# Optimization experiments

Hardware: AMD Instinct MI355X
Metric: run time of the kernel (lower is better)

Reference implementation:

```python
import jax, jax.numpy as jnp
import numpy as np
import math

B, S, DIM, QK, HID = 20, 500, 300, 128, 600  # batch, seq, model dim, query_key_dim, hidden_dim
ROT = 32          # rotary dim = min(32, query_key_dim)
NB, MD = 32, 128  # T5 bias num_buckets, max_distance


def _layernorm(x, g, b, eps=1e-5):
    mu = jnp.mean(x, axis=-1, keepdims=True)
    var = jnp.var(x, axis=-1, keepdims=True)
    return (x - mu) / jnp.sqrt(var + eps) * g + b


def _rowquant(y, axis):
    # per-row (or per-col) symmetric int4-range quant used by the module:
    # scale = max|y|/15, clamp to [-15,15], truncate toward zero (torch .to(int8))
    s = jnp.max(jnp.abs(y), axis=axis, keepdims=True) / 15.0
    yq = jnp.trunc(jnp.clip(y / s, -15.0, 15.0))
    return yq, s


def _rotary(t):
    # rotary-embedding-torch: rotate first ROT features, interleaved pairs
    inv_freq = 1.0 / (10000.0 ** (jnp.arange(0, ROT, 2, dtype=jnp.float32) / ROT))  # [ROT/2]
    pos = jnp.arange(S, dtype=jnp.float32)
    freqs = jnp.repeat(pos[:, None] * inv_freq[None, :], 2, axis=-1)  # [S, ROT]
    cos, sin = jnp.cos(freqs), jnp.sin(freqs)
    tr, tp = t[..., :ROT], t[..., ROT:]
    x1, x2 = tr[..., 0::2], tr[..., 1::2]
    rot_half = jnp.stack([-x2, x1], axis=-1).reshape(tr.shape)
    return jnp.concatenate([tr * cos + rot_half * sin, tp], axis=-1)


def _t5_bias(rel_emb):
    # non-causal T5 relative position bucket, num_buckets=32 -> halved to 16
    pos = jnp.arange(S)
    n = -(pos[None, :] - pos[:, None])  # -(k_pos - q_pos)
    nb = NB // 2
    ret = (n < 0).astype(jnp.int32) * nb
    n = jnp.abs(n)
    max_exact = nb // 2
    is_small = n < max_exact
    n_safe = jnp.maximum(n, 1).astype(jnp.float32)
    val_large = max_exact + (jnp.log(n_safe / max_exact) / math.log(MD / max_exact) * (nb - max_exact)).astype(jnp.int32)
    val_large = jnp.minimum(val_large, nb - 1)
    bucket = ret + jnp.where(is_small, n, val_large)  # [S, S]
    return rel_emb[bucket, 0] * math.sqrt(QK)


def setup_inputs() -> dict:
    key = jax.random.key(0)
    ks = jax.random.split(key, 16)
    nrm = lambda i, shp, std=0.02: jax.random.normal(ks[i], shp, jnp.float32) * std
    uni = lambda i, shp, lo, hi: jax.random.uniform(ks[i], shp, jnp.float32, lo, hi)
    return {
        "x": jax.random.normal(ks[0], (B, S, DIM), jnp.float32),
        "norm_gamma": jnp.ones((DIM,), jnp.float32),
        "norm_beta": jnp.zeros((DIM,), jnp.float32),
        "Wh": nrm(1, (2 * HID, DIM)),
        "bh": jnp.zeros((2 * HID,), jnp.float32),
        "Wqk": nrm(2, (QK, DIM)),
        "bqk": jnp.zeros((QK,), jnp.float32),
        "os_gamma": nrm(3, (2, QK)),
        "os_beta": jnp.zeros((2, QK), jnp.float32),
        "Wo": nrm(4, (DIM, HID)),
        "bo": jnp.zeros((DIM,), jnp.float32),
        "rel_emb": nrm(5, (NB, 1), 0.1),
        "qk_s": uni(6, (DIM,), 0.5, 1.5),
        "hidden_s": uni(7, (DIM,), 0.5, 1.5),
        "out_s": uni(8, (HID,), 0.5, 1.5),
        "hidden_params": uni(9, (2 * HID,), 0.01, 0.05),
        "qk_params": uni(10, (QK,), 0.01, 0.05),
        "out_params": uni(11, (DIM,), 0.01, 0.05),
    }


def reference(x, norm_gamma, norm_beta, Wh, bh, Wqk, bqk, os_gamma, os_beta, Wo, bo,
              rel_emb, qk_s, hidden_s, out_s, hidden_params, qk_params, out_params):
    normed = _layernorm(x, norm_gamma, norm_beta)
    # token shift on first half of features
    half = DIM // 2
    x_shift = jnp.pad(normed[..., :half], ((0, 0), (1, 0), (0, 0)))[:, :S, :]
    normed = jnp.concatenate([x_shift, normed[..., half:]], axis=-1)

    # per-weight-column pre-scale then per-row int8 quant
    xq_q, sq = _rowquant(normed / qk_s, axis=-1)      # sq [B,S,1]
    xh_q, sh = _rowquant(normed / hidden_s, axis=-1)  # sh [B,S,1]

    # to_hidden: Linear + SiLU, then dequant outer(row_scale, hidden_params)
    v_gate = jax.nn.silu(xh_q @ Wh.T + bh) * (sh * hidden_params)  # [B,S,2*HID]
    v, gate = v_gate[..., :HID], v_gate[..., HID:]

    qk = jax.nn.silu(xq_q @ Wqk.T + bqk) * (sq * qk_params)  # [B,S,QK]
    q = qk * os_gamma[0] + os_beta[0]
    k = qk * os_gamma[1] + os_beta[1]
    q, k = _rotary(q), _rotary(k)

    qq, qs = _rowquant(q, axis=-1)
    kq, ks_ = _rowquant(k, axis=-1)
    sim = jnp.trunc(jnp.einsum('bid,bjd->bij', qq, kq)) * qs * jnp.swapaxes(ks_, 1, 2)
    sim = sim + _t5_bias(rel_emb)

    attn = jnp.square(jax.nn.relu(sim / S))
    aq, as_ = _rowquant(attn, axis=-1)  # as_ [B,S,1]
    vq, vs = _rowquant(v, axis=1)       # vs [B,1,HID] (per-column)
    out = jnp.trunc(jnp.einsum('bij,bjd->bid', aq, vq)) * as_ * vs  # [B,S,HID]

    out = out * gate / out_s
    oq, osc = _rowquant(out, axis=-1)
    out = (oq @ Wo.T + bo) * (osc * out_params)  # [B,S,DIM]
    return out + x
```

## Files before the change

### kernel.cpp

```cpp
#include <hip/hip_runtime.h>
#include <math.h>

#define B_   20
#define S_   500
#define DIM_ 300
#define QK_  128
#define HID_ 600
#define NROW (B_ * S_)

typedef int   v4i  __attribute__((ext_vector_type(4)));

__device__ __forceinline__ unsigned short f32_to_bf16(float f) {
  unsigned int u = __float_as_uint(f);
  unsigned int r = (u + 0x7FFFu + ((u >> 16) & 1u)) >> 16;
  return (unsigned short)r;
}
__device__ __forceinline__ float bf16_to_f32(unsigned short s) {
  return __uint_as_float(((unsigned int)s) << 16);
}

__device__ __forceinline__ float quant15(float y, float s) {
  return truncf(fminf(fmaxf(__fdiv_rn(y, s), -15.f), 15.f));
}

__global__ __launch_bounds__(256) void k_prep_ln(
    const float* __restrict__ x,
    const float* __restrict__ g, const float* __restrict__ b,
    const float* __restrict__ qk_s, const float* __restrict__ hidden_s,
    signed char* __restrict__ xq8, signed char* __restrict__ xh8,
    float* __restrict__ sq, float* __restrict__ sh,
    const float* __restrict__ rel_emb, float* __restrict__ dbias,
    const float* __restrict__ Wh, signed char* __restrict__ q1h, float* __restrict__ s1h,
    const float* __restrict__ Wo, signed char* __restrict__ q1o, float* __restrict__ s1o,
    const float* __restrict__ Wqk, signed char* __restrict__ q1k, float* __restrict__ s1k) {
  int blk = blockIdx.x;
  int tid = threadIdx.x;
  int lane = tid & 63;
  if (blk < 2500) {
    int row = blk * 4 + (tid >> 6);
    if (row >= NROW) return;
    bool hasp = (row % S_) > 0;
    const float* xr = x + (size_t)row * DIM_;
    const float* xpr = x + (size_t)(row - 1) * DIM_;
    float xc[5], xp[5];
    #pragma unroll
    for (int i = 0; i < 5; ++i) {
      int c = lane + i * 64;
      xc[i] = (c < DIM_) ? xr[c] : 0.f;
      xp[i] = (hasp && c < DIM_) ? xpr[c] : 0.f;
    }
    float sc = 0.f, sp = 0.f;
    #pragma unroll
    for (int i = 0; i < 5; ++i) { sc += xc[i]; sp += xp[i]; }
    #pragma unroll
    for (int off = 1; off < 64; off <<= 1) {
      sc += __shfl_xor(sc, off);
      sp += __shfl_xor(sp, off);
    }
    float mu_c = sc / (float)DIM_, mu_p = sp / (float)DIM_;
    float vc = 0.f, vp = 0.f;
    #pragma unroll
    for (int i = 0; i < 5; ++i) {
      int c = lane + i * 64;
      if (c < DIM_) {
        float dc = xc[i] - mu_c; vc += dc * dc;
        float dp = xp[i] - mu_p; vp += dp * dp;
      }
    }
    #pragma unroll
    for (int off = 1; off < 64; off <<= 1) {
      vc += __shfl_xor(vc, off);
      vp += __shfl_xor(vp, off);
    }
    float den_c = sqrtf(vc / (float)DIM_ + 1e-5f);
    float den_p = sqrtf(vp / (float)DIM_ + 1e-5f);
    float yq[5], yh[5];
    float mq = 0.f, mh = 0.f;
    #pragma unroll
    for (int i = 0; i < 5; ++i) {
      int c = lane + i * 64;
      if (c < DIM_) {
        float src;
        if (c < DIM_ / 2)
          src = hasp ? __fdiv_rn(xp[i] - mu_p, den_p) * g[c] + b[c] : 0.f;
        else
          src = __fdiv_rn(xc[i] - mu_c, den_c) * g[c] + b[c];
        yq[i] = __fdiv_rn(src, qk_s[c]);
        yh[i] = __fdiv_rn(src, hidden_s[c]);
        mq = fmaxf(mq, fabsf(yq[i]));
        mh = fmaxf(mh, fabsf(yh[i]));
      }
    }
    #pragma unroll
    for (int off = 1; off < 64; off <<= 1) {
      mq = fmaxf(mq, __shfl_xor(mq, off));
      mh = fmaxf(mh, __shfl_xor(mh, off));
    }
    float sqv = mq / 15.0f, shv = mh / 15.0f;
    if (lane == 0) { sq[row] = sqv; sh[row] = shv; }
    #pragma unroll
    for (int i = 0; i < 5; ++i) {
      int c = lane + i * 64;
      if (c < DIM_) {
        xq8[(size_t)row * 320 + c] = (signed char)quant15(yq[i], sqv);
        xh8[(size_t)row * 320 + c] = (signed char)quant15(yh[i], shv);
      } else if (c < 320) {
        xq8[(size_t)row * 320 + c] = 0;
        xh8[(size_t)row * 320 + c] = 0;
      }
    }
    return;
  }
  int jidx = (blk - 2500) * 4 + (tid >> 6);
  if (jidx >= 1744) return;
  if (jidx < 16) {
    int idx = jidx * 64 + lane;
    int dd = idx - 512;
    int ret = (dd < 0) ? 16 : 0;
    int n = dd < 0 ? -dd : dd;
    int v;
    if (n < 8)       v = n;
    else if (n < 12) v = 8;
    else if (n < 16) v = 9;
    else if (n < 23) v = 10;
    else if (n < 32) v = 11;
    else if (n < 46) v = 12;
    else if (n < 64) v = 13;
    else if (n < 91) v = 14;
    else             v = 15;
    dbias[idx] = __fmul_rn(rel_emb[ret + v], 11.313708498984761f);
    return;
  }
  const float* src; signed char* q1; float* s1;
  int j, C, CP;
  if (jidx < 1296)      { j = jidx - 16;   src = Wh;  q1 = q1h; s1 = s1h; C = DIM_; CP = 320; }
  else if (jidx < 1616) { j = jidx - 1296; src = Wo;  q1 = q1o; s1 = s1o; C = HID_; CP = 640; }
  else                  { j = jidx - 1616; src = Wqk; q1 = q1k; s1 = s1k; C = DIM_; CP = 320; }
  float m = 0.f;
  for (int k = lane; k < C; k += 64) m = fmaxf(m, fabsf(src[(size_t)j * C + k]));
  #pragma unroll
  for (int off = 1; off < 64; off <<= 1) m = fmaxf(m, __shfl_xor(m, off));
  float s1v = m / 127.0f;
  float s1inv = s1v > 0.f ? 1.0f / s1v : 0.f;
  if (lane == 0) s1[j] = s1v;
  for (int k = lane; k < CP; k += 64) {
    float wv = (k < C) ? src[(size_t)j * C + k] : 0.f;
    float q1f = fminf(fmaxf(rintf(wv * s1inv), -127.f), 127.f);
    q1[(size_t)j * CP + k] = (signed char)q1f;
  }
}

__global__ __launch_bounds__(512) void k_hqk(
    const signed char* __restrict__ xh8p, const signed char* __restrict__ xq8p,
    const float* __restrict__ sh, const float* __restrict__ sq,
    const signed char* __restrict__ q1h, const float* __restrict__ s1h,
    const float* __restrict__ bh, const float* __restrict__ hp,
    unsigned short* __restrict__ v16, unsigned short* __restrict__ gate16,
    int* __restrict__ vsmax,
    const signed char* __restrict__ q1k, const float* __restrict__ s1k,
    const float* __restrict__ bqk, const float* __restrict__ qkp,
    const float* __restrict__ osg, const float* __restrict__ osb,
    signed char* __restrict__ qq8, signed char* __restrict__ kq2,
    float* __restrict__ qs, float* __restrict__ ks) {
  __shared__ __align__(16) signed char smem[33792];
  int blk = blockIdx.x;
  int tid = threadIdx.x;
  int w = tid >> 6, l = tid & 63, g = l >> 4, ln = l & 15;
  v4i zero = {0, 0, 0, 0};
  int rxor = ((g ^ ((ln >> 1) & 3)) * 16);

  if (blk < 760) {
    int j0 = (blk % 19) * 64;
    int i0 = (blk / 19) * 256;
    int wm = w >> 1, wn = w & 1;
    signed char* a_lds  = smem;
    signed char* b1_lds = smem + 16384;
    unsigned short* st  = (unsigned short*)smem;

    int r0 = tid >> 2, ch0 = tid & 3;
    int r1 = r0 + 128;
    int koff0 = ((ch0 ^ ((r0 >> 1) & 3)) * 16);
    int koff1 = ((ch0 ^ ((r1 >> 1) & 3)) * 16);
    int ga0 = i0 + r0; if (ga0 >= NROW) ga0 = NROW - 1;
    int ga1 = i0 + r1; if (ga1 >= NROW) ga1 = NROW - 1;
    const signed char* srcA0 = xh8p + (size_t)ga0 * 320 + koff0;
    const signed char* srcA1 = xh8p + (size_t)ga1 * 320 + koff1;
    bool hasB = tid < 256;
    int br = (tid & 255) >> 2, bch = tid & 3;
    int bkoff = ((bch ^ ((br >> 1) & 3)) * 16);
    const signed char* srcB = q1h + (size_t)(j0 + br) * 320 + bkoff;

    v4i pa0 = *(const v4i*)srcA0;
    v4i pa1 = *(const v4i*)srcA1;
    v4i pb = hasB ? *(const v4i*)srcB : zero;

    v4i acc1[4][2];
    #pragma unroll
    for (int sl = 0; sl < 4; ++sl)
      #pragma unroll
      for (int t = 0; t < 2; ++t) acc1[sl][t] = zero;

    for (int st_i = 0; st_i < 5; ++st_i) {
      *(v4i*)(a_lds + tid * 16)        = pa0;
      *(v4i*)(a_lds + 8192 + tid * 16) = pa1;
      if (hasB) *(v4i*)(b1_lds + tid * 16) = pb;
      __syncthreads();
      if (st_i < 4) {
        int k0 = (st_i + 1) * 64;
        pa0 = *(const v4i*)(srcA0 + k0);
        pa1 = *(const v4i*)(srcA1 + k0);
        if (hasB) pb = *(const v4i*)(srcB + k0);
      }
      v4i af[4];
      #pragma unroll
      for (int sl = 0; sl < 4; ++sl)
        af[sl] = *(const v4i*)(a_lds + (wm * 64 + sl * 16 + ln) * 64 + rxor);
      #pragma unroll
      for (int t = 0; t < 2; ++t) {
        int boff = (wn * 32 + t * 16 + ln) * 64 + rxor;
        v4i b1 = *(const v4i*)(b1_lds + boff);
        #pragma unroll
        for (int sl = 0; sl < 4; ++sl)
          acc1[sl][t] = __builtin_amdgcn_mfma_i32_16x16x64_i8(af[sl], b1, acc1[sl][t], 0, 0, 0);
      }
      __syncthreads();
    }
    int rbase = i0 + wm * 64;
    int b0 = rbase / S_;
    int bbound = (b0 + 1) * S_;
    int rtop = rbase + 63; if (rtop >= NROW) rtop = NROW - 1;
    int b1i = rtop / S_;
    #pragma unroll
    for (int t = 0; t < 2; ++t) {
      int col = j0 + wn * 32 + t * 16 + ln;
      int cl = wn * 32 + t * 16 + ln;
      if (col < 2 * HID_) {
        float s1v = s1h[col], bc = bh[col], hpc = hp[col];
        bool isv = col < HID_;
        float m0 = 0.f, m1 = 0.f;
        #pragma unroll
        for (int sl = 0; sl < 4; ++sl) {
          #pragma unroll
          for (int r = 0; r < 4; ++r) {
            int grow = rbase + sl * 16 + g * 4 + r;
            if (grow < NROW) {
              float z = s1v * (float)acc1[sl][t][r] + bc;
              float sig = 1.0f / (1.0f + __expf(-z));
              float val = __fmul_rn(z * sig, __fmul_rn(sh[grow], hpc));
              unsigned short hv = f32_to_bf16(val);
              st[(wm * 64 + sl * 16 + g * 4 + r) * 66 + cl] = hv;
              if (isv) {
                float vr = fabsf(bf16_to_f32(hv));
                if (grow < bbound) m0 = fmaxf(m0, vr);
                else               m1 = fmaxf(m1, vr);
              }
            }
          }
        }
        if (isv) {
          atomicMax(&vsmax[b0 * 640 + col], __float_as_int(m0));
          if (b1i != b0) atomicMax(&vsmax[b1i * 640 + col], __float_as_int(m1));
        }
      }
    }
    __syncthreads();
    for (int idx = tid; idx < 2048; idx += 512) {
      int r = idx >> 3, seg = idx & 7;
      int grow = i0 + r;
      int col0 = j0 + seg * 8;
      if (grow < NROW && col0 < 2 * HID_) {
        const unsigned int* sp = (const unsigned int*)(st + r * 66 + seg * 8);
        v4i pk;
        pk[0] = sp[0]; pk[1] = sp[1]; pk[2] = sp[2]; pk[3] = sp[3];
        if (col0 < HID_)
          *(v4i*)(v16 + (size_t)grow * HID_ + col0) = pk;
        else
          *(v4i*)(gate16 + (size_t)grow * HID_ + (col0 - HID_)) = pk;
      }
    }
    return;
  }
  {
    int i0 = (blk - 760) * 128;
    signed char* a_lds  = smem;
    signed char* b1_lds = smem + 8192;
    float* freqs = (float*)(smem + 16384);
    if (tid < 32) {
      double e = (double)(tid & ~1) / 32.0;
      freqs[tid] = (float)(1.0 / pow(10000.0, e));
    }
    int r = tid >> 2, ch = tid & 3;
    int koff = ((ch ^ ((r >> 1) & 3)) * 16);
    int ga = i0 + r; if (ga >= NROW) ga = NROW - 1;
    const signed char* srcA  = xq8p + (size_t)ga * 320 + koff;
    const signed char* srcB1 = q1k + (size_t)r * 320 + koff;
    v4i pa  = *(const v4i*)srcA;
    v4i pb1 = *(const v4i*)srcB1;
    v4i acc1[8];
    #pragma unroll
    for (int t = 0; t < 8; ++t) acc1[t] = zero;
    for (int st = 0; st < 5; ++st) {
      *(v4i*)(a_lds + tid * 16)  = pa;
      *(v4i*)(b1_lds + tid * 16) = pb1;
      __syncthreads();
      if (st < 4) {
        int k0 = (st + 1) * 64;
        pa  = *(const v4i*)(srcA + k0);
        pb1 = *(const v4i*)(srcB1 + k0);
      }
      v4i af = *(const v4i*)(a_lds + (w * 16 + ln) * 64 + rxor);
      #pragma unroll
      for (int t = 0; t < 8; ++t) {
        int boff = (t * 16 + ln) * 64 + rxor;
        v4i b1 = *(const v4i*)(b1_lds + boff);
        acc1[t] = __builtin_amdgcn_mfma_i32_16x16x64_i8(af, b1, acc1[t], 0, 0, 0);
      }
      __syncthreads();
    }
    int growr[4]; float sqr[4];
    #pragma unroll
    for (int r2 = 0; r2 < 4; ++r2) {
      growr[r2] = i0 + w * 16 + g * 4 + r2;
      int gc = growr[r2] < NROW ? growr[r2] : NROW - 1;
      sqr[r2] = sq[gc];
    }
    float qv[8][4], kv[8][4];
    #pragma unroll
    for (int t = 0; t < 8; ++t) {
      int c = t * 16 + ln;
      float s1v = s1k[c], bc = bqk[c], qkpc = qkp[c];
      float g0 = osg[c], g1 = osg[QK_ + c], b0 = osb[c], b1v = osb[QK_ + c];
      #pragma unroll
      for (int r2 = 0; r2 < 4; ++r2) {
        float z = s1v * (float)acc1[t][r2] + bc;
        float sig = 1.0f / (1.0f + expf(-z));
        float qkv = __fmul_rn(z * sig, __fmul_rn(sqr[r2], qkpc));
        qv[t][r2] = __fadd_rn(__fmul_rn(qkv, g0), b0);
        kv[t][r2] = __fadd_rn(__fmul_rn(qkv, g1), b1v);
      }
    }
    #pragma unroll
    for (int t = 0; t < 2; ++t) {
      float inv = freqs[t * 16 + ln];
      #pragma unroll
      for (int r2 = 0; r2 < 4; ++r2) {
        int pos = growr[r2] % S_;
        float fr = __fmul_rn((float)pos, inv);
        float cs = cosf(fr), sn = sinf(fr);
        float qo = __shfl_xor(qv[t][r2], 1);
        float ko = __shfl_xor(kv[t][r2], 1);
        float rq = ((ln & 1) == 0) ? -qo : qo;
        float rk = ((ln & 1) == 0) ? -ko : ko;
        qv[t][r2] = __fadd_rn(__fmul_rn(qv[t][r2], cs), __fmul_rn(rq, sn));
        kv[t][r2] = __fadd_rn(__fmul_rn(kv[t][r2], cs), __fmul_rn(rk, sn));
      }
    }
    float qsv[4], ksv[4];
    #pragma unroll
    for (int r2 = 0; r2 < 4; ++r2) {
      float mq = 0.f, mk = 0.f;
      #pragma unroll
      for (int t = 0; t < 8; ++t) {
        mq = fmaxf(mq, fabsf(qv[t][r2]));
        mk = fmaxf(mk, fabsf(kv[t][r2]));
      }
      #pragma unroll
      for (int off = 1; off < 16; off <<= 1) {
        mq = fmaxf(mq, __shfl_xor(mq, off));
        mk = fmaxf(mk, __shfl_xor(mk, off));
      }
      qsv[r2] = mq / 15.0f; ksv[r2] = mk / 15.0f;
      if (ln == 0 && growr[r2] < NROW) { qs[growr[r2]] = qsv[r2]; ks[growr[r2]] = ksv[r2]; }
    }
    #pragma unroll
    for (int t = 0; t < 8; ++t) {
      int c = t * 16 + ln;
      #pragma unroll
      for (int r2 = 0; r2 < 4; ++r2) {
        if (growr[r2] < NROW) {
          qq8[(size_t)growr[r2] * QK_ + c] = (signed char)quant15(qv[t][r2], qsv[r2]);
          int bb = growr[r2] / S_, ss = growr[r2] % S_;
          kq2[(((size_t)bb * 2 + (c >> 6)) * 512 + ss) * 64 + (c & 63)] =
              (signed char)quant15(kv[t][r2], ksv[r2]);
        }
      }
    }
  }
}

__global__ __launch_bounds__(512) void k_simpv(
    const signed char* __restrict__ qq8, const signed char* __restrict__ kq2,
    const float* __restrict__ qs, const float* __restrict__ ks,
    const float* __restrict__ dbias,
    const signed char* __restrict__ vqt2, const float* __restrict__ vg,
    const unsigned short* __restrict__ gate16,
    signed char* __restrict__ oq8, float* __restrict__ osc) {
  int i0 = blockIdx.x * 16;
  int b = blockIdx.y;
  int tid = threadIdx.x;
  int w = tid >> 6, l = tid & 63, g = l >> 4, ln = l & 15;
  __shared__ __align__(16) signed char q_lds[16 * 144];
  __shared__ __align__(16) signed char p_lds[16 * 528];
  __shared__ float db[1024];
  __shared__ int rowmax[16];
  if (tid < 128) {
    int r = tid >> 3, ww = tid & 7;
    *(v4i*)(q_lds + r * 144 + ww * 16) =
        *(const v4i*)(qq8 + ((size_t)(b * S_ + i0 + r)) * QK_ + ww * 16);
  }
  for (int idx = tid; idx < 1024; idx += 512) db[idx] = dbias[idx];
  if (tid < 16) rowmax[tid] = 0;
  __syncthreads();
  v4i acc[4];
  v4i zero = {0, 0, 0, 0};
  #pragma unroll
  for (int t = 0; t < 4; ++t) acc[t] = zero;
  #pragma unroll
  for (int kk = 0; kk < 2; ++kk) {
    v4i afrag = *(const v4i*)(q_lds + ln * 144 + kk * 64 + g * 16);
    #pragma unroll
    for (int t = 0; t < 4; ++t) {
      int j0 = (w * 4 + t) * 16;
      v4i bfrag = *(const v4i*)(kq2 + (((size_t)b * 2 + kk) * 512 + j0 + ln) * 64 + g * 16);
      acc[t] = __builtin_amdgcn_mfma_i32_16x16x64_i8(afrag, bfrag, acc[t], 0, 0, 0);
    }
  }
  float qsr[4];
  #pragma unroll
  for (int r = 0; r < 4; ++r) qsr[r] = qs[b * S_ + i0 + g * 4 + r];
  float rm[4] = {0.f, 0.f, 0.f, 0.f};
  #pragma unroll
  for (int t = 0; t < 4; ++t) {
    int j = (w * 4 + t) * 16 + ln;
    bool jv = j < S_;
    float ksv = ks[b * S_ + j];
    #pragma unroll
    for (int r = 0; r < 4; ++r) {
      int ip = i0 + g * 4 + r;
      float av = 0.f;
      if (jv) {
        float simv = __fmul_rn(__fmul_rn((float)acc[t][r], qsr[r]), ksv);
        simv = __fadd_rn(simv, db[ip - j + 512]);
        float rr = fmaxf(__fmul_rn(simv, 0.002f), 0.f);
        av = __fmul_rn(rr, rr);
      }
      rm[r] = fmaxf(rm[r], av);
      acc[t][r] = __float_as_int(av);
    }
  }
  #pragma unroll
  for (int r = 0; r < 4; ++r) atomicMax(&rowmax[g * 4 + r], __float_as_int(rm[r]));
  __syncthreads();
  float asr[4], rinv[4];
  #pragma unroll
  for (int r = 0; r < 4; ++r) {
    asr[r] = __int_as_float(rowmax[g * 4 + r]) / 15.0f;
    rinv[r] = __fdiv_rn(1.0f, asr[r]);
  }
  #pragma unroll
  for (int t = 0; t < 4; ++t) {
    int j = (w * 4 + t) * 16 + ln;
    #pragma unroll
    for (int r = 0; r < 4; ++r) {
      float y = __int_as_float(acc[t][r]);
      float q = truncf(fminf(fmaxf(__fmul_rn(y, rinv[r]), -15.f), 15.f));
      p_lds[(g * 4 + r) * 528 + j] = (signed char)q;
    }
  }
  __syncthreads();
  if (tid < 16) rowmax[tid] = 0;
  __syncthreads();
  v4i pacc[5];
  #pragma unroll
  for (int t = 0; t < 5; ++t) pacc[t] = zero;
  for (int kk = 0; kk < 8; ++kk) {
    v4i afrag = *(const v4i*)(p_lds + ln * 528 + kk * 64 + g * 16);
    const signed char* bbase = vqt2 + (((size_t)b * 8 + kk) * 640) * 64 + g * 16;
    #pragma unroll
    for (int t = 0; t < 5; ++t) {
      int d = (w * 5 + t) * 16 + ln;
      v4i bfrag = *(const v4i*)(bbase + (size_t)d * 64);
      pacc[t] = __builtin_amdgcn_mfma_i32_16x16x64_i8(afrag, bfrag, pacc[t], 0, 0, 0);
    }
  }
  float rm2[4] = {0.f, 0.f, 0.f, 0.f};
  #pragma unroll
  for (int t = 0; t < 5; ++t) {
    int d = (w * 5 + t) * 16 + ln;
    bool dv = d < HID_;
    float vgv = vg[b * 640 + d];
    #pragma unroll
    for (int r = 0; r < 4; ++r) {
      float o = 0.f;
      if (dv) {
        float gt = bf16_to_f32(gate16[((size_t)(b * S_ + i0 + g * 4 + r)) * HID_ + d]);
        o = __fmul_rn(__fmul_rn(__fmul_rn((float)pacc[t][r], asr[r]), vgv), gt);
      }
      rm2[r] = fmaxf(rm2[r], fabsf(o));
      pacc[t][r] = __float_as_int(o);
    }
  }
  #pragma unroll
  for (int r = 0; r < 4; ++r) atomicMax(&rowmax[g * 4 + r], __float_as_int(rm2[r]));
  __syncthreads();
  float orinv[4];
  #pragma unroll
  for (int r = 0; r < 4; ++r) {
    float osr = __int_as_float(rowmax[g * 4 + r]) / 15.0f;
    orinv[r] = __fdiv_rn(1.0f, osr);
  }
  #pragma unroll
  for (int t = 0; t < 5; ++t) {
    int d = (w * 5 + t) * 16 + ln;
    #pragma unroll
    for (int r = 0; r < 4; ++r) {
      int il = i0 + g * 4 + r;
      if (il < S_) {
        signed char valc = 0;
        if (d < HID_) {
          float q = truncf(fminf(fmaxf(
              __fmul_rn(__int_as_float(pacc[t][r]), orinv[r]), -15.f), 15.f));
          valc = (signed char)q;
        }
        oq8[((size_t)b * S_ + il) * 640 + d] = valc;
      }
    }
  }
  if (tid < 16 && i0 + tid < S_)
    osc[b * S_ + i0 + tid] = __int_as_float(rowmax[tid]) / 15.0f;
}

__global__ __launch_bounds__(256) void k_vq2(const unsigned short* __restrict__ v16,
                                             const int* __restrict__ vsmax,
                                             const float* __restrict__ out_s,
                                             signed char* __restrict__ vqt2,
                                             float* __restrict__ vg) {
  int b = blockIdx.z;
  int s0 = blockIdx.x * 64;
  int d0 = blockIdx.y * 64;
  __shared__ float tile[64][65];
  int tid = threadIdx.x;
  int dj = tid & 63, si4 = tid >> 6;
  #pragma unroll
  for (int it = 0; it < 16; ++it) {
    int s = s0 + it * 4 + si4;
    int d = d0 + dj;
    float val = 0.f;
    if (s < S_ && d < HID_) val = bf16_to_f32(v16[((size_t)b * S_ + s) * HID_ + d]);
    tile[it * 4 + si4][dj] = val;
  }
  if (blockIdx.x == 0 && tid < 64) {
    int d = d0 + tid;
    float vsv = __int_as_float(vsmax[b * 640 + d]) / 15.0f;
    vg[b * 640 + d] = (d < HID_) ? __fdiv_rn(vsv, out_s[d]) : 0.f;
  }
  __syncthreads();
  int dd = tid >> 2, seg = tid & 3;
  int d = d0 + dd;
  int kk = s0 >> 6;
  v4i pack = {0, 0, 0, 0};
  if (d < HID_) {
    float vsv = __int_as_float(vsmax[b * 640 + d]) / 15.0f;
    signed char* pc = (signed char*)&pack;
    #pragma unroll
    for (int e = 0; e < 16; ++e)
      pc[e] = (signed char)quant15(tile[seg * 16 + e][dd], vsv);
  }
  *(v4i*)(vqt2 + ((((size_t)b * 8 + kk) * 640) + d) * 64 + seg * 16) = pack;
}

__global__ __launch_bounds__(256) void k_final(
    const signed char* __restrict__ oq8p, const float* __restrict__ osc,
    const signed char* __restrict__ q1o, const float* __restrict__ s1o,
    const float* __restrict__ bo, const float* __restrict__ op,
    const float* __restrict__ x, float* __restrict__ out) {
  int i0 = blockIdx.x * 128;
  int j0 = blockIdx.y * 64;
  int tid = threadIdx.x;
  int w = tid >> 6, l = tid & 63, g = l >> 4, ln = l & 15;
  int wm = w >> 1, wn = w & 1;
  __shared__ __align__(16) signed char a_lds[128 * 64];
  __shared__ __align__(16) signed char b1_lds[64 * 64];

  int arow0 = tid >> 2;
  int xorb = (((tid & 3) ^ ((tid >> 3) & 3)) * 16);
  int ga0 = i0 + arow0;       if (ga0 >= NROW) ga0 = NROW - 1;
  int ga1 = i0 + arow0 + 64;  if (ga1 >= NROW) ga1 = NROW - 1;
  int gcol = j0 + arow0;
  const signed char* srcA0 = oq8p + (size_t)ga0 * 640 + xorb;
  const signed char* srcA1 = oq8p + (size_t)ga1 * 640 + xorb;
  const signed char* srcB1 = q1o + (size_t)gcol * 640 + xorb;

  v4i pa0 = *(const v4i*)(srcA0);
  v4i pa1 = *(const v4i*)(srcA1);
  v4i pb1 = *(const v4i*)(srcB1);

  int rxor = ((g ^ ((ln >> 1) & 3)) * 16);
  v4i acc1[4][2];
  v4i zero = {0, 0, 0, 0};
  #pragma unroll
  for (int sl = 0; sl < 4; ++sl)
    #pragma unroll
    for (int t = 0; t < 2; ++t) acc1[sl][t] = zero;

  for (int st = 0; st < 10; ++st) {
    *(v4i*)(a_lds + tid * 16)        = pa0;
    *(v4i*)(a_lds + 4096 + tid * 16) = pa1;
    *(v4i*)(b1_lds + tid * 16)       = pb1;
    __syncthreads();
    if (st < 9) {
      int k0 = (st + 1) * 64;
      pa0 = *(const v4i*)(srcA0 + k0);
      pa1 = *(const v4i*)(srcA1 + k0);
      pb1 = *(const v4i*)(srcB1 + k0);
    }
    v4i af[4];
    #pragma unroll
    for (int sl = 0; sl < 4; ++sl)
      af[sl] = *(const v4i*)(a_lds + (wm * 64 + sl * 16 + ln) * 64 + rxor);
    #pragma unroll
    for (int t = 0; t < 2; ++t) {
      int boff = (wn * 32 + t * 16 + ln) * 64 + rxor;
      v4i b1 = *(const v4i*)(b1_lds + boff);
      #pragma unroll
      for (int sl = 0; sl < 4; ++sl)
        acc1[sl][t] = __builtin_amdgcn_mfma_i32_16x16x64_i8(af[sl], b1, acc1[sl][t], 0, 0, 0);
    }
    __syncthreads();
  }
  #pragma unroll
  for (int t = 0; t < 2; ++t) {
    int col = j0 + wn * 32 + t * 16 + ln;
    if (col < DIM_) {
      float s1v = s1o[col], bc = bo[col], opc = op[col];
      #pragma unroll
      for (int sl = 0; sl < 4; ++sl) {
        #pragma unroll
        for (int r = 0; r < 4; ++r) {
          int grow = i0 + wm * 64 + sl * 16 + g * 4 + r;
          if (grow < NROW) {
            float z = s1v * (float)acc1[sl][t][r] + bc;
            float tval = __fmul_rn(osc[grow], opc);
            out[(size_t)grow * DIM_ + col] =
                __fmul_rn(z, tval) + x[(size_t)grow * DIM_ + col];
          }
        }
      }
    }
  }
}

extern "C" void kernel_launch(void* const* d_in, const int* in_sizes, int n_in,
                              void* d_out, int out_size, void* d_ws, size_t ws_size,
                              hipStream_t stream) {
  const float* x        = (const float*)d_in[0];
  const float* ng       = (const float*)d_in[1];
  const float* nbt      = (const float*)d_in[2];
  const float* Wh       = (const float*)d_in[3];
  const float* bh       = (const float*)d_in[4];
  const float* Wqk      = (const float*)d_in[5];
  const float* bqk      = (const float*)d_in[6];
  const float* osg      = (const float*)d_in[7];
  const float* osb      = (const float*)d_in[8];
  const float* Wo       = (const float*)d_in[9];
  const float* bo       = (const float*)d_in[10];
  const float* rel      = (const float*)d_in[11];
  const float* qk_s     = (const float*)d_in[12];
  const float* hidden_s = (const float*)d_in[13];
  const float* out_s    = (const float*)d_in[14];
  const float* hp       = (const float*)d_in[15];
  const float* qkp      = (const float*)d_in[16];
  const float* op       = (const float*)d_in[17];
  float* out = (float*)d_out;

  char* ws = (char*)d_ws;
  size_t off = 0;
  auto alloc = [&](size_t bytes) {
    void* p = ws + off;
    off += (bytes + 255) & ~(size_t)255;
    return p;
  };
  signed char* xq8    = (signed char*)alloc((size_t)(NROW + 128) * 320);
  signed char* xh8    = (signed char*)alloc((size_t)(NROW + 256) * 320);
  float*       sq     = (float*)      alloc((size_t)(NROW + 256) * 4);
  float*       sh     = (float*)      alloc((size_t)(NROW + 256) * 4);
  unsigned short* v16   = (unsigned short*)alloc((size_t)(NROW + 256) * HID_ * 2);
  unsigned short* gate16= (unsigned short*)alloc((size_t)(NROW + 256) * HID_ * 2);
  signed char* qq8    = (signed char*)alloc((size_t)(NROW + 128) * QK_);
  signed char* kq2    = (signed char*)alloc((size_t)B_ * 2 * 512 * 64);
  float*       qs     = (float*)      alloc((size_t)(NROW + 128) * 4);
  float*       ks     = (float*)      alloc((size_t)(NROW + 128) * 4);
  signed char* vqt2   = (signed char*)alloc((size_t)B_ * 8 * 640 * 64);
  float*       vg     = (float*)      alloc((size_t)B_ * 640 * 4);
  int*         vsmax  = (int*)        alloc((size_t)B_ * 640 * 4);
  signed char* oq8    = (signed char*)alloc((size_t)(NROW + 128) * 640);
  float*       osc    = (float*)      alloc((size_t)(NROW + 128) * 4);
  float*       dbias  = (float*)      alloc((size_t)1024 * 4);
  signed char* q1h    = (signed char*)alloc((size_t)1280 * 320);
  float*       s1h    = (float*)      alloc((size_t)1280 * 4);
  signed char* q1o    = (signed char*)alloc((size_t)320 * 640);
  float*       s1o    = (float*)      alloc((size_t)320 * 4);
  signed char* q1k    = (signed char*)alloc((size_t)QK_ * 320);
  float*       s1k    = (float*)      alloc((size_t)QK_ * 4);


  k_prep_ln<<<2936, 256, 0, stream>>>(x, ng, nbt, qk_s, hidden_s, xq8, xh8, sq, sh,
                                      rel, dbias, Wh, q1h, s1h, Wo, q1o, s1o,
                                      Wqk, q1k, s1k);
  k_hqk<<<839, 512, 0, stream>>>(xh8, xq8, sh, sq, q1h, s1h, bh, hp,
                                 v16, gate16, vsmax,
                                 q1k, s1k, bqk, qkp, osg, osb,
                                 qq8, kq2, qs, ks);
  k_vq2<<<dim3(8, 10, B_), 256, 0, stream>>>(v16, vsmax, out_s, vqt2, vg);
  k_simpv<<<dim3(32, B_), 512, 0, stream>>>(qq8, kq2, qs, ks, dbias, vqt2, vg,
                                            gate16, oq8, osc);
  k_final<<<dim3(79, 5), 256, 0, stream>>>(oq8, osc, q1o, s1o, bo, op, x, out);
}
```

Baseline: 128.6 us.

## Split fused hidden/QK projection kernel into separate launches with smaller QK tiles

The combined k_hqk kernel, which branched on block index between the hidden projection and the QK projection, is split into two kernels. k_hidden keeps the 256x64 tile on a 2D grid. k_qk now uses 64-row tiles with 256 threads and 157 blocks instead of 79 blocks of 128 rows, which gives the QK path more parallelism and uses less LDS per block. The cost is an extra kernel launch and the loss of running both branches concurrently inside one grid.

```diff
diff --git a/kernel.cpp b/kernel.cpp
--- a/kernel.cpp
+++ b/kernel.cpp
@@ -150,239 +150,242 @@
   }
 }
 
-__global__ __launch_bounds__(512) void k_hqk(
-    const signed char* __restrict__ xh8p, const signed char* __restrict__ xq8p,
-    const float* __restrict__ sh, const float* __restrict__ sq,
+__global__ __launch_bounds__(512) void k_hidden(
+    const signed char* __restrict__ xh8p, const float* __restrict__ sh,
     const signed char* __restrict__ q1h, const float* __restrict__ s1h,
     const float* __restrict__ bh, const float* __restrict__ hp,
     unsigned short* __restrict__ v16, unsigned short* __restrict__ gate16,
-    int* __restrict__ vsmax,
+    int* __restrict__ vsmax) {
+  int j0 = blockIdx.x * 64;
+  int i0 = blockIdx.y * 256;
+  int tid = threadIdx.x;
+  int w = tid >> 6, l = tid & 63, g = l >> 4, ln = l & 15;
+  int wm = w >> 1, wn = w & 1;
+  __shared__ __align__(16) signed char smem[33792];
+  signed char* a_lds  = smem;
+  signed char* b1_lds = smem + 16384;
+  unsigned short* st  = (unsigned short*)smem;
+
+  int r0 = tid >> 2, ch0 = tid & 3;
+  int r1 = r0 + 128;
+  int koff0 = ((ch0 ^ ((r0 >> 1) & 3)) * 16);
+  int koff1 = ((ch0 ^ ((r1 >> 1) & 3)) * 16);
+  int ga0 = i0 + r0; if (ga0 >= NROW) ga0 = NROW - 1;
+  int ga1 = i0 + r1; if (ga1 >= NROW) ga1 = NROW - 1;
+  const signed char* srcA0 = xh8p + (size_t)ga0 * 320 + koff0;
+  const signed char* srcA1 = xh8p + (size_t)ga1 * 320 + koff1;
+  bool hasB = tid < 256;
+  int br = (tid & 255) >> 2, bch = tid & 3;
+  int bkoff = ((bch ^ ((br >> 1) & 3)) * 16);
+  const signed char* srcB = q1h + (size_t)(j0 + br) * 320 + bkoff;
+
+  v4i pa0 = *(const v4i*)srcA0;
+  v4i pa1 = *(const v4i*)srcA1;
+  v4i zero = {0, 0, 0, 0};
+  v4i pb = hasB ? *(const v4i*)srcB : zero;
+
+  int rxor = ((g ^ ((ln >> 1) & 3)) * 16);
+  v4i acc1[4][2];
+  #pragma unroll
+  for (int sl = 0; sl < 4; ++sl)
+    #pragma unroll
+    for (int t = 0; t < 2; ++t) acc1[sl][t] = zero;
+
+  for (int st_i = 0; st_i < 5; ++st_i) {
+    *(v4i*)(a_lds + tid * 16)        = pa0;
+    *(v4i*)(a_lds + 8192 + tid * 16) = pa1;
+    if (hasB) *(v4i*)(b1_lds + tid * 16) = pb;
+    __syncthreads();
+    if (st_i < 4) {
+      int k0 = (st_i + 1) * 64;
+      pa0 = *(const v4i*)(srcA0 + k0);
+      pa1 = *(const v4i*)(srcA1 + k0);
+      if (hasB) pb = *(const v4i*)(srcB + k0);
+    }
+    v4i af[4];
+    #pragma unroll
+    for (int sl = 0; sl < 4; ++sl)
+      af[sl] = *(const v4i*)(a_lds + (wm * 64 + sl * 16 + ln) * 64 + rxor);
+    #pragma unroll
+    for (int t = 0; t < 2; ++t) {
+      int boff = (wn * 32 + t * 16 + ln) * 64 + rxor;
+      v4i b1 = *(const v4i*)(b1_lds + boff);
+      #pragma unroll
+      for (int sl = 0; sl < 4; ++sl)
+        acc1[sl][t] = __builtin_amdgcn_mfma_i32_16x16x64_i8(af[sl], b1, acc1[sl][t], 0, 0, 0);
+    }
+    __syncthreads();
+  }
+  int rbase = i0 + wm * 64;
+  int b0 = rbase / S_;
+  int bbound = (b0 + 1) * S_;
+  int rtop = rbase + 63; if (rtop >= NROW) rtop = NROW - 1;
+  int b1i = rtop / S_;
+  #pragma unroll
+  for (int t = 0; t < 2; ++t) {
+    int col = j0 + wn * 32 + t * 16 + ln;
+    int cl = wn * 32 + t * 16 + ln;
+    if (col < 2 * HID_) {
+      float s1v = s1h[col], bc = bh[col], hpc = hp[col];
+      bool isv = col < HID_;
+      float m0 = 0.f, m1 = 0.f;
+      #pragma unroll
+      for (int sl = 0; sl < 4; ++sl) {
+        #pragma unroll
+        for (int r = 0; r < 4; ++r) {
+          int grow = rbase + sl * 16 + g * 4 + r;
+          if (grow < NROW) {
+            float z = s1v * (float)acc1[sl][t][r] + bc;
+            float sig = 1.0f / (1.0f + __expf(-z));
+            float val = __fmul_rn(z * sig, __fmul_rn(sh[grow], hpc));
+            unsigned short hv = f32_to_bf16(val);
+            st[(wm * 64 + sl * 16 + g * 4 + r) * 66 + cl] = hv;
+            if (isv) {
+              float vr = fabsf(bf16_to_f32(hv));
+              if (grow < bbound) m0 = fmaxf(m0, vr);
+              else               m1 = fmaxf(m1, vr);
+            }
+          }
+        }
+      }
+      if (isv) {
+        atomicMax(&vsmax[b0 * 640 + col], __float_as_int(m0));
+        if (b1i != b0) atomicMax(&vsmax[b1i * 640 + col], __float_as_int(m1));
+      }
+    }
+  }
+  __syncthreads();
+  for (int idx = tid; idx < 2048; idx += 512) {
+    int r = idx >> 3, seg = idx & 7;
+    int grow = i0 + r;
+    int col0 = j0 + seg * 8;
+    if (grow < NROW && col0 < 2 * HID_) {
+      const unsigned int* sp = (const unsigned int*)(st + r * 66 + seg * 8);
+      v4i pk;
+      pk[0] = sp[0]; pk[1] = sp[1]; pk[2] = sp[2]; pk[3] = sp[3];
+      if (col0 < HID_)
+        *(v4i*)(v16 + (size_t)grow * HID_ + col0) = pk;
+      else
+        *(v4i*)(gate16 + (size_t)grow * HID_ + (col0 - HID_)) = pk;
+    }
+  }
+}
+
+__global__ __launch_bounds__(256) void k_qk(
+    const signed char* __restrict__ xq8p, const float* __restrict__ sq,
     const signed char* __restrict__ q1k, const float* __restrict__ s1k,
     const float* __restrict__ bqk, const float* __restrict__ qkp,
     const float* __restrict__ osg, const float* __restrict__ osb,
     signed char* __restrict__ qq8, signed char* __restrict__ kq2,
     float* __restrict__ qs, float* __restrict__ ks) {
-  __shared__ __align__(16) signed char smem[33792];
-  int blk = blockIdx.x;
+  int i0 = blockIdx.x * 64;
   int tid = threadIdx.x;
   int w = tid >> 6, l = tid & 63, g = l >> 4, ln = l & 15;
+  __shared__ __align__(16) signed char a_lds[64 * 64];
+  __shared__ __align__(16) signed char b1_lds[128 * 64];
+  __shared__ float freqs[32];
+  if (tid < 32) {
+    double e = (double)(tid & ~1) / 32.0;
+    freqs[tid] = (float)(1.0 / pow(10000.0, e));
+  }
+  int arow = tid >> 2;
+  int xorb = (((tid & 3) ^ ((tid >> 3) & 3)) * 16);
+  int ga = i0 + arow; if (ga >= NROW) ga = NROW - 1;
+  const signed char* srcA   = xq8p + (size_t)ga * 320 + xorb;
+  const signed char* srcB1a = q1k + (size_t)arow * 320 + xorb;
+  const signed char* srcB1b = q1k + (size_t)(64 + arow) * 320 + xorb;
+  v4i pa   = *(const v4i*)srcA;
+  v4i pb1a = *(const v4i*)srcB1a, pb1b = *(const v4i*)srcB1b;
+  int rxor = ((g ^ ((ln >> 1) & 3)) * 16);
+  v4i acc1[8];
   v4i zero = {0, 0, 0, 0};
-  int rxor = ((g ^ ((ln >> 1) & 3)) * 16);
-
-  if (blk < 760) {
-    int j0 = (blk % 19) * 64;
-    int i0 = (blk / 19) * 256;
-    int wm = w >> 1, wn = w & 1;
-    signed char* a_lds  = smem;
-    signed char* b1_lds = smem + 16384;
-    unsigned short* st  = (unsigned short*)smem;
-
-    int r0 = tid >> 2, ch0 = tid & 3;
-    int r1 = r0 + 128;
-    int koff0 = ((ch0 ^ ((r0 >> 1) & 3)) * 16);
-    int koff1 = ((ch0 ^ ((r1 >> 1) & 3)) * 16);
-    int ga0 = i0 + r0; if (ga0 >= NROW) ga0 = NROW - 1;
-    int ga1 = i0 + r1; if (ga1 >= NROW) ga1 = NROW - 1;
-    const signed char* srcA0 = xh8p + (size_t)ga0 * 320 + koff0;
-    const signed char* srcA1 = xh8p + (size_t)ga1 * 320 + koff1;
-    bool hasB = tid < 256;
-    int br = (tid & 255) >> 2, bch = tid & 3;
-    int bkoff = ((bch ^ ((br >> 1) & 3)) * 16);
-    const signed char* srcB = q1h + (size_t)(j0 + br) * 320 + bkoff;
-
-    v4i pa0 = *(const v4i*)srcA0;
-    v4i pa1 = *(const v4i*)srcA1;
-    v4i pb = hasB ? *(const v4i*)srcB : zero;
-
-    v4i acc1[4][2];
-    #pragma unroll
-    for (int sl = 0; sl < 4; ++sl)
-      #pragma unroll
-      for (int t = 0; t < 2; ++t) acc1[sl][t] = zero;
-
-    for (int st_i = 0; st_i < 5; ++st_i) {
-      *(v4i*)(a_lds + tid * 16)        = pa0;
-      *(v4i*)(a_lds + 8192 + tid * 16) = pa1;
-      if (hasB) *(v4i*)(b1_lds + tid * 16) = pb;
-      __syncthreads();
-      if (st_i < 4) {
-        int k0 = (st_i + 1) * 64;
-        pa0 = *(const v4i*)(srcA0 + k0);
-        pa1 = *(const v4i*)(srcA1 + k0);
-        if (hasB) pb = *(const v4i*)(srcB + k0);
-      }
-      v4i af[4];
-      #pragma unroll
-      for (int sl = 0; sl < 4; ++sl)
-        af[sl] = *(const v4i*)(a_lds + (wm * 64 + sl * 16 + ln) * 64 + rxor);
-      #pragma unroll
-      for (int t = 0; t < 2; ++t) {
-        int boff = (wn * 32 + t * 16 + ln) * 64 + rxor;
-        v4i b1 = *(const v4i*)(b1_lds + boff);
-        #pragma unroll
-        for (int sl = 0; sl < 4; ++sl)
-          acc1[sl][t] = __builtin_amdgcn_mfma_i32_16x16x64_i8(af[sl], b1, acc1[sl][t], 0, 0, 0);
-      }
-      __syncthreads();
-    }
-    int rbase = i0 + wm * 64;
-    int b0 = rbase / S_;
-    int bbound = (b0 + 1) * S_;
-    int rtop = rbase + 63; if (rtop >= NROW) rtop = NROW - 1;
-    int b1i = rtop / S_;
-    #pragma unroll
-    for (int t = 0; t < 2; ++t) {
-      int col = j0 + wn * 32 + t * 16 + ln;
-      int cl = wn * 32 + t * 16 + ln;
-      if (col < 2 * HID_) {
-        float s1v = s1h[col], bc = bh[col], hpc = hp[col];
-        bool isv = col < HID_;
-        float m0 = 0.f, m1 = 0.f;
-        #pragma unroll
-        for (int sl = 0; sl < 4; ++sl) {
-          #pragma unroll
-          for (int r = 0; r < 4; ++r) {
-            int grow = rbase + sl * 16 + g * 4 + r;
-            if (grow < NROW) {
-              float z = s1v * (float)acc1[sl][t][r] + bc;
-              float sig = 1.0f / (1.0f + __expf(-z));
-              float val = __fmul_rn(z * sig, __fmul_rn(sh[grow], hpc));
-              unsigned short hv = f32_to_bf16(val);
-              st[(wm * 64 + sl * 16 + g * 4 + r) * 66 + cl] = hv;
-              if (isv) {
-                float vr = fabsf(bf16_to_f32(hv));
-                if (grow < bbound) m0 = fmaxf(m0, vr);
-                else               m1 = fmaxf(m1, vr);
-              }
-            }
-          }
-        }
-        if (isv) {
-          atomicMax(&vsmax[b0 * 640 + col], __float_as_int(m0));
-          if (b1i != b0) atomicMax(&vsmax[b1i * 640 + col], __float_as_int(m1));
-        }
-      }
-    }
+  #pragma unroll
+  for (int t = 0; t < 8; ++t) acc1[t] = zero;
+  for (int st = 0; st < 5; ++st) {
+    *(v4i*)(a_lds + tid * 16)         = pa;
+    *(v4i*)(b1_lds + tid * 16)        = pb1a;
+    *(v4i*)(b1_lds + 4096 + tid * 16) = pb1b;
     __syncthreads();
-    for (int idx = tid; idx < 2048; idx += 512) {
-      int r = idx >> 3, seg = idx & 7;
-      int grow = i0 + r;
-      int col0 = j0 + seg * 8;
-      if (grow < NROW && col0 < 2 * HID_) {
-        const unsigned int* sp = (const unsigned int*)(st + r * 66 + seg * 8);
-        v4i pk;
-        pk[0] = sp[0]; pk[1] = sp[1]; pk[2] = sp[2]; pk[3] = sp[3];
-        if (col0 < HID_)
-          *(v4i*)(v16 + (size_t)grow * HID_ + col0) = pk;
-        else
-          *(v4i*)(gate16 + (size_t)grow * HID_ + (col0 - HID_)) = pk;
-      }
-    }
-    return;
-  }
-  {
-    int i0 = (blk - 760) * 128;
-    signed char* a_lds  = smem;
-    signed char* b1_lds = smem + 8192;
-    float* freqs = (float*)(smem + 16384);
-    if (tid < 32) {
-      double e = (double)(tid & ~1) / 32.0;
-      freqs[tid] = (float)(1.0 / pow(10000.0, e));
-    }
-    int r = tid >> 2, ch = tid & 3;
-    int koff = ((ch ^ ((r >> 1) & 3)) * 16);
-    int ga = i0 + r; if (ga >= NROW) ga = NROW - 1;
-    const signed char* srcA  = xq8p + (size_t)ga * 320 + koff;
-    const signed char* srcB1 = q1k + (size_t)r * 320 + koff;
-    v4i pa  = *(const v4i*)srcA;
-    v4i pb1 = *(const v4i*)srcB1;
-    v4i acc1[8];
-    #pragma unroll
-    for (int t = 0; t < 8; ++t) acc1[t] = zero;
-    for (int st = 0; st < 5; ++st) {
-      *(v4i*)(a_lds + tid * 16)  = pa;
-      *(v4i*)(b1_lds + tid * 16) = pb1;
-      __syncthreads();
-      if (st < 4) {
-        int k0 = (st + 1) * 64;
-        pa  = *(const v4i*)(srcA + k0);
-        pb1 = *(const v4i*)(srcB1 + k0);
-      }
-      v4i af = *(const v4i*)(a_lds + (w * 16 + ln) * 64 + rxor);
-      #pragma unroll
-      for (int t = 0; t < 8; ++t) {
-        int boff = (t * 16 + ln) * 64 + rxor;
-        v4i b1 = *(const v4i*)(b1_lds + boff);
-        acc1[t] = __builtin_amdgcn_mfma_i32_16x16x64_i8(af, b1, acc1[t], 0, 0, 0);
-      }
-      __syncthreads();
-    }
-    int growr[4]; float sqr[4];
-    #pragma unroll
-    for (int r2 = 0; r2 < 4; ++r2) {
-      growr[r2] = i0 + w * 16 + g * 4 + r2;
-      int gc = growr[r2] < NROW ? growr[r2] : NROW - 1;
-      sqr[r2] = sq[gc];
-    }
-    float qv[8][4], kv[8][4];
+    if (st < 4) {
+      int k0 = (st + 1) * 64;
+      pa   = *(const v4i*)(srcA + k0);
+      pb1a = *(const v4i*)(srcB1a + k0);
+      pb1b = *(const v4i*)(srcB1b + k0);
+    }
+    v4i af = *(const v4i*)(a_lds + (w * 16 + ln) * 64 + rxor);
     #pragma unroll
     for (int t = 0; t < 8; ++t) {
-      int c = t * 16 + ln;
-      float s1v = s1k[c], bc = bqk[c], qkpc = qkp[c];
-      float g0 = osg[c], g1 = osg[QK_ + c], b0 = osb[c], b1v = osb[QK_ + c];
-      #pragma unroll
-      for (int r2 = 0; r2 < 4; ++r2) {
-        float z = s1v * (float)acc1[t][r2] + bc;
-        float sig = 1.0f / (1.0f + expf(-z));
-        float qkv = __fmul_rn(z * sig, __fmul_rn(sqr[r2], qkpc));
-        qv[t][r2] = __fadd_rn(__fmul_rn(qkv, g0), b0);
-        kv[t][r2] = __fadd_rn(__fmul_rn(qkv, g1), b1v);
-      }
-    }
-    #pragma unroll
-    for (int t = 0; t < 2; ++t) {
-      float inv = freqs[t * 16 + ln];
-      #pragma unroll
-      for (int r2 = 0; r2 < 4; ++r2) {
-        int pos = growr[r2] % S_;
-        float fr = __fmul_rn((float)pos, inv);
-        float cs = cosf(fr), sn = sinf(fr);
-        float qo = __shfl_xor(qv[t][r2], 1);
-        float ko = __shfl_xor(kv[t][r2], 1);
-        float rq = ((ln & 1) == 0) ? -qo : qo;
-        float rk = ((ln & 1) == 0) ? -ko : ko;
-        qv[t][r2] = __fadd_rn(__fmul_rn(qv[t][r2], cs), __fmul_rn(rq, sn));
-        kv[t][r2] = __fadd_rn(__fmul_rn(kv[t][r2], cs), __fmul_rn(rk, sn));
-      }
-    }
-    float qsv[4], ksv[4];
-    #pragma unroll
-    for (int r2 = 0; r2 < 4; ++r2) {
-      float mq = 0.f, mk = 0.f;
-      #pragma unroll
-      for (int t = 0; t < 8; ++t) {
-        mq = fmaxf(mq, fabsf(qv[t][r2]));
-        mk = fmaxf(mk, fabsf(kv[t][r2]));
-      }
-      #pragma unroll
-      for (int off = 1; off < 16; off <<= 1) {
-        mq = fmaxf(mq, __shfl_xor(mq, off));
-        mk = fmaxf(mk, __shfl_xor(mk, off));
-      }
-      qsv[r2] = mq / 15.0f; ksv[r2] = mk / 15.0f;
-      if (ln == 0 && growr[r2] < NROW) { qs[growr[r2]] = qsv[r2]; ks[growr[r2]] = ksv[r2]; }
-    }
+      int boff = (t * 16 + ln) * 64 + rxor;
+      v4i b1 = *(const v4i*)(b1_lds + boff);
+      acc1[t] = __builtin_amdgcn_mfma_i32_16x16x64_i8(af, b1, acc1[t], 0, 0, 0);
+    }
+    __syncthreads();
+  }
+  int growr[4]; float sqr[4];
+  #pragma unroll
+  for (int r = 0; r < 4; ++r) {
+    growr[r] = i0 + w * 16 + g * 4 + r;
+    int gc = growr[r] < NROW ? growr[r] : NROW - 1;
+    sqr[r] = sq[gc];
+  }
+  float qv[8][4], kv[8][4];
+  #pragma unroll
+  for (int t = 0; t < 8; ++t) {
+    int c = t * 16 + ln;
+    float s1v = s1k[c], bc = bqk[c], qkpc = qkp[c];
+    float g0 = osg[c], g1 = osg[QK_ + c], b0 = osb[c], b1v = osb[QK_ + c];
+    #pragma unroll
+    for (int r = 0; r < 4; ++r) {
+      float z = s1v * (float)acc1[t][r] + bc;
+      float sig = 1.0f / (1.0f + expf(-z));
+      float qkv = __fmul_rn(z * sig, __fmul_rn(sqr[r], qkpc));
+      qv[t][r] = __fadd_rn(__fmul_rn(qkv, g0), b0);
+      kv[t][r] = __fadd_rn(__fmul_rn(qkv, g1), b1v);
+    }
+  }
+  #pragma unroll
+  for (int t = 0; t < 2; ++t) {
+    float inv = freqs[t * 16 + ln];
+    #pragma unroll
+    for (int r = 0; r < 4; ++r) {
+      int pos = growr[r] % S_;
+      float fr = __fmul_rn((float)pos, inv);
+      float cs = cosf(fr), sn = sinf(fr);
+      float qo = __shfl_xor(qv[t][r], 1);
+      float ko = __shfl_xor(kv[t][r], 1);
+      float rq = ((ln & 1) == 0) ? -qo : qo;
+      float rk = ((ln & 1) == 0) ? -ko : ko;
+      qv[t][r] = __fadd_rn(__fmul_rn(qv[t][r], cs), __fmul_rn(rq, sn));
+      kv[t][r] = __fadd_rn(__fmul_rn(kv[t][r], cs), __fmul_rn(rk, sn));
+    }
+  }
+  float qsv[4], ksv[4];
+  #pragma unroll
+  for (int r = 0; r < 4; ++r) {
+    float mq = 0.f, mk = 0.f;
     #pragma unroll
     for (int t = 0; t < 8; ++t) {
-      int c = t * 16 + ln;
-      #pragma unroll
-      for (int r2 = 0; r2 < 4; ++r2) {
-        if (growr[r2] < NROW) {
-          qq8[(size_t)growr[r2] * QK_ + c] = (signed char)quant15(qv[t][r2], qsv[r2]);
-          int bb = growr[r2] / S_, ss = growr[r2] % S_;
-          kq2[(((size_t)bb * 2 + (c >> 6)) * 512 + ss) * 64 + (c & 63)] =
-              (signed char)quant15(kv[t][r2], ksv[r2]);
-        }
+      mq = fmaxf(mq, fabsf(qv[t][r]));
+      mk = fmaxf(mk, fabsf(kv[t][r]));
+    }
+    #pragma unroll
+    for (int off = 1; off < 16; off <<= 1) {
+      mq = fmaxf(mq, __shfl_xor(mq, off));
+      mk = fmaxf(mk, __shfl_xor(mk, off));
+    }
+    qsv[r] = mq / 15.0f; ksv[r] = mk / 15.0f;
+    if (ln == 0 && growr[r] < NROW) { qs[growr[r]] = qsv[r]; ks[growr[r]] = ksv[r]; }
+  }
+  #pragma unroll
+  for (int t = 0; t < 8; ++t) {
+    int c = t * 16 + ln;
+    #pragma unroll
+    for (int r = 0; r < 4; ++r) {
+      if (growr[r] < NROW) {
+        qq8[(size_t)growr[r] * QK_ + c] = (signed char)quant15(qv[t][r], qsv[r]);
+        int bb = growr[r] / S_, ss = growr[r] % S_;
+        kq2[(((size_t)bb * 2 + (c >> 6)) * 512 + ss) * 64 + (c & 63)] =
+            (signed char)quant15(kv[t][r], ksv[r]);
       }
     }
   }
@@ -707,10 +710,10 @@
   k_prep_ln<<<2936, 256, 0, stream>>>(x, ng, nbt, qk_s, hidden_s, xq8, xh8, sq, sh,
                                       rel, dbias, Wh, q1h, s1h, Wo, q1o, s1o,
                                       Wqk, q1k, s1k);
-  k_hqk<<<839, 512, 0, stream>>>(xh8, xq8, sh, sq, q1h, s1h, bh, hp,
-                                 v16, gate16, vsmax,
-                                 q1k, s1k, bqk, qkp, osg, osb,
-                                 qq8, kq2, qs, ks);
+  k_hidden<<<dim3(19, 40), 512, 0, stream>>>(xh8, sh, q1h, s1h, bh, hp,
+                                             v16, gate16, vsmax);
+  k_qk<<<157, 256, 0, stream>>>(xq8, sq, q1k, s1k, bqk, qkp, osg, osb,
+                                qq8, kq2, qs, ks);
   k_vq2<<<dim3(8, 10, B_), 256, 0, stream>>>(v16, vsmax, out_s, vqt2, vg);
   k_simpv<<<dim3(32, B_), 512, 0, stream>>>(qq8, kq2, qs, ks, dbias, vqt2, vg,
                                             gate16, oq8, osc);
```

Measured after the change: 124.7 us. 3.0% less time.
